# Kernel tuning notes

Hardware: AMD Instinct MI355X
Metric: run time of the kernel (lower is better)

## Reference

```python
import jax, jax.numpy as jnp
import numpy as np

H = 1024
HEADS = 16
FFN = 2048
EPS = 1e-5


def _layernorm(x, g, b):
    mu = jnp.mean(x, axis=-1, keepdims=True)
    var = jnp.mean(jnp.square(x - mu), axis=-1, keepdims=True)
    return (x - mu) * jax.lax.rsqrt(var + EPS) * g + b


def setup_inputs() -> dict:
    key = jax.random.key(0)
    ks = jax.random.split(key, 8)
    N, L = 4, 1024
    s = 1.0 / np.sqrt(H)
    inp = {
        "src_hidden": jax.random.normal(ks[0], (N, L, H), dtype=jnp.float32),
        "src_mask": jnp.ones((N, L), dtype=jnp.int32),
        "Wq": jax.random.normal(ks[1], (H, H), dtype=jnp.float32) * s,
        "bq": jnp.zeros((H,), jnp.float32),
        "Wk": jax.random.normal(ks[2], (H, H), dtype=jnp.float32) * s,
        "bk": jnp.zeros((H,), jnp.float32),
        "Wv": jax.random.normal(ks[3], (H, H), dtype=jnp.float32) * s,
        "bv": jnp.zeros((H,), jnp.float32),
        "Wo": jax.random.normal(ks[4], (H, H), dtype=jnp.float32) * s,
        "bo": jnp.zeros((H,), jnp.float32),
        "ln1_g": jnp.ones((H,), jnp.float32),
        "ln1_b": jnp.zeros((H,), jnp.float32),
        "W1": jax.random.normal(ks[5], (H, FFN), dtype=jnp.float32) * s,
        "b1": jnp.zeros((FFN,), jnp.float32),
        "W2": jax.random.normal(ks[6], (FFN, H), dtype=jnp.float32) * (1.0 / np.sqrt(FFN)),
        "b2": jnp.zeros((H,), jnp.float32),
        "ln2_g": jnp.ones((H,), jnp.float32),
        "ln2_b": jnp.zeros((H,), jnp.float32),
    }
    return inp


def reference(src_hidden, src_mask, Wq, bq, Wk, bk, Wv, bv, Wo, bo,
              ln1_g, ln1_b, W1, b1, W2, b2, ln2_g, ln2_b):
    N, L, _ = src_hidden.shape
    d = H // HEADS
    scale = 1.0 / np.sqrt(H)  # applied to BOTH Q and K, as in the original
    # NOTE: head split is a plain reshape (view), faithful to the original code
    Q = ((src_hidden @ Wq + bq).reshape(N, HEADS, L, d)) * scale
    K = ((src_hidden @ Wk + bk).reshape(N, HEADS, L, d)) * scale
    V = (src_hidden @ Wv + bv).reshape(N, HEADS, L, d)
    sims = jnp.einsum('nhid,nhjd->nhij', Q, K)  # (N, heads, L, L)
    mask = src_mask[:, None, None, :]  # (N,1,1,L) broadcasts over heads and query dim
    sims = jnp.where(mask == 0, -jnp.inf, sims)
    attn = jax.nn.softmax(sims, axis=-1)
    ctx = jnp.einsum('nhij,nhjd->nhid', attn, V)
    concats = ctx.reshape(N, L, H)
    hid = concats @ Wo + bo
    x1 = _layernorm(hid, ln1_g, ln1_b) + hid
    ffn = jax.nn.relu(x1 @ W1 + b1) @ W2 + b2  # dropout is identity in eval
    out = _layernorm(ffn, ln2_g, ln2_b) + ffn
    return (out, src_mask)
```

## Files before the change

kernel.cpp:

```cpp
#include <hip/hip_runtime.h>
#include <math.h>

#define H 1024
#define HEADS 16
#define DH 64
#define FFN_DIM 2048
#define EPS 1e-5f
#define NB 4
#define LL 1024
#define M_ROWS 4096

typedef __attribute__((ext_vector_type(8))) short bf16x8;
typedef __attribute__((ext_vector_type(4))) float f32x4;

__device__ __forceinline__ ushort f2bf(float x) {
    union { float f; unsigned u; } c; c.f = x;
    unsigned u = c.u;
    u += 0x7FFFu + ((u >> 16) & 1u);
    return (ushort)(u >> 16);
}

#define GLL(gp, lp)                                                         \
    __builtin_amdgcn_global_load_lds(                                       \
        (const __attribute__((address_space(1))) void*)(gp),                \
        (__attribute__((address_space(3))) void*)(lp), 16, 0, 0)

#define WAITV4() asm volatile("s_waitcnt vmcnt(4)" ::: "memory")
#define WAITV2() asm volatile("s_waitcnt vmcnt(2)" ::: "memory")
#define WAITV0() asm volatile("s_waitcnt vmcnt(0)" ::: "memory")
#define BAR() __builtin_amdgcn_s_barrier()

__global__ __launch_bounds__(512, 6)
void gemm_bf16(const ushort* __restrict__ A, const ushort* __restrict__ Bt,
               const float* __restrict__ bias, float* __restrict__ Cf0,
               float* __restrict__ Cf1, ushort* __restrict__ Cb,
               int M, int N, int K, int relu, int qkv)
{
    __shared__ ushort As[3][128 * 32];
    __shared__ ushort Bs[3][128 * 32];
    const int tid = threadIdx.x;
    const int l = tid & 63, w = tid >> 6;
    const int wr = w >> 2, wc = w & 3;
    const int g = l >> 4, c0 = l & 15;
    const int brow = blockIdx.y * 128, bcol = blockIdx.x * 128;
    const int z = blockIdx.z;
    const int Ksub = K / gridDim.z;
    const int NS = Ksub >> 5;

    const ushort* Abase = A + (size_t)brow * K + (size_t)z * Ksub;
    const ushort* Bbase = Bt + (size_t)bcol * K + (size_t)z * Ksub;

    f32x4 acc[4][2];
    #pragma unroll
    for (int mi = 0; mi < 4; ++mi)
        #pragma unroll
        for (int ni = 0; ni < 2; ++ni)
            acc[mi][ni] = (f32x4)0.0f;

    auto stage = [&](int buf, int k0) {
        const int row = tid >> 2, cp = tid & 3;
        const int c = cp ^ ((row >> 1) & 3);
        const ushort* ga = Abase + (size_t)row * K + k0 + c * 8;
        const ushort* gb = Bbase + (size_t)row * K + k0 + c * 8;
        ushort* la = As[buf] + (size_t)w * 512;
        ushort* lb = Bs[buf] + (size_t)w * 512;
        GLL(ga, la);
        GLL(gb, lb);
    };

    stage(0, 0);
    stage(1, 32);
    int scur = 0;
    for (int t = 0; t < NS; ++t) {
        int snext = scur + 2; if (snext >= 3) snext -= 3;
        if (t + 2 < NS) stage(snext, (t + 2) << 5);
        if (t < NS - 2)       WAITV4();
        else if (t == NS - 2) WAITV2();
        else                  WAITV0();
        BAR();

        bf16x8 af[4], bf[2];
        #pragma unroll
        for (int mi = 0; mi < 4; ++mi) {
            const int row = wr * 64 + mi * 16 + c0;
            const int cc = g ^ ((row >> 1) & 3);
            af[mi] = *(const bf16x8*)&As[scur][row * 32 + cc * 8];
        }
        #pragma unroll
        for (int ni = 0; ni < 2; ++ni) {
            const int row = wc * 32 + ni * 16 + c0;
            const int cc = g ^ ((row >> 1) & 3);
            bf[ni] = *(const bf16x8*)&Bs[scur][row * 32 + cc * 8];
        }
        __builtin_amdgcn_s_setprio(1);
        #pragma unroll
        for (int mi = 0; mi < 4; ++mi)
            #pragma unroll
            for (int ni = 0; ni < 2; ++ni)
                acc[mi][ni] = __builtin_amdgcn_mfma_f32_16x16x32_bf16(
                    af[mi], bf[ni], acc[mi][ni], 0, 0, 0);
        __builtin_amdgcn_s_setprio(0);
        BAR();
        scur = scur + 1 == 3 ? 0 : scur + 1;
    }

    float* Cf = (z == 0) ? Cf0 : Cf1;
    const int colg0 = bcol + wc * 32 + c0;
    const int rbase = brow + wr * 64 + (g << 2);
    const int seg   = qkv ? (bcol >> 10) : 0;
    const int Nw    = qkv ? 1024 : N;
    ushort* outb    = qkv ? (Cb + (size_t)seg * 4194304u) : Cb;
    #pragma unroll
    for (int ni = 0; ni < 2; ++ni) {
        const int colg = colg0 + ni * 16;
        const int colw = qkv ? (colg & 1023) : colg;
        const float bv = (z == 0) ? bias[colg] : 0.0f;
        #pragma unroll
        for (int mi = 0; mi < 4; ++mi) {
            #pragma unroll
            for (int j = 0; j < 4; ++j) {
                float v = acc[mi][ni][j] + bv;
                if (relu) v = fmaxf(v, 0.0f);
                const size_t off = (size_t)(rbase + mi * 16 + j) * Nw + colw;
                if (Cf) Cf[off] = v;
                if (Cb) outb[off] = f2bf(v);
            }
        }
    }
}

__global__ __launch_bounds__(256)
void transpose_qkvo(const float* __restrict__ Wq, const float* __restrict__ Wk,
                    const float* __restrict__ Wv, const float* __restrict__ Wo,
                    ushort* __restrict__ Dq, ushort* __restrict__ Dk,
                    ushort* __restrict__ Dv, ushort* __restrict__ Do_)
{
    const float* W; ushort* D; float sc;
    switch (blockIdx.z) {
        case 0:  W = Wq; D = Dq;  sc = 0.03125f; break;
        case 1:  W = Wk; D = Dk;  sc = 0.03125f; break;
        case 2:  W = Wv; D = Dv;  sc = 1.0f;     break;
        default: W = Wo; D = Do_; sc = 1.0f;     break;
    }
    __shared__ float t[32][33];
    const int n0 = blockIdx.x * 32, k0 = blockIdx.y * 32;
    const int tx = threadIdx.x & 31, ty = threadIdx.x >> 5;
    #pragma unroll
    for (int r = 0; r < 4; ++r)
        t[ty + r * 8][tx] = W[(size_t)(k0 + ty + r * 8) * H + n0 + tx];
    __syncthreads();
    #pragma unroll
    for (int r = 0; r < 4; ++r)
        D[(size_t)(n0 + ty + r * 8) * H + k0 + tx] =
            f2bf(t[tx][ty + r * 8] * sc);
}

__global__ __launch_bounds__(256)
void transpose_to_bf16(const float* __restrict__ W, ushort* __restrict__ Wt,
                       int K, int N, float scale)
{
    __shared__ float t[32][33];
    const int n0 = blockIdx.x * 32, k0 = blockIdx.y * 32;
    const int tx = threadIdx.x & 31, ty = threadIdx.x >> 5;
    #pragma unroll
    for (int r = 0; r < 4; ++r)
        t[ty + r * 8][tx] = W[(size_t)(k0 + ty + r * 8) * N + n0 + tx];
    __syncthreads();
    #pragma unroll
    for (int r = 0; r < 4; ++r)
        Wt[(size_t)(n0 + ty + r * 8) * K + k0 + tx] =
            f2bf(t[tx][ty + r * 8] * scale);
}

__global__ __launch_bounds__(256)
void transpose_v(const ushort* __restrict__ V, ushort* __restrict__ Vt)
{
    const int nh = blockIdx.y, jt = blockIdx.x;
    const size_t base = (size_t)nh << 16;
    __shared__ ushort t[64][68];
    const int tid = threadIdx.x;
    #pragma unroll
    for (int pass = 0; pass < 4; ++pass) {
        const int j = pass * 16 + (tid >> 4);
        const int d0 = (tid & 15) * 4;
        ushort4 v = *(const ushort4*)&V[base + (size_t)(jt * 64 + j) * 64 + d0];
        t[d0 + 0][j] = v.x; t[d0 + 1][j] = v.y;
        t[d0 + 2][j] = v.z; t[d0 + 3][j] = v.w;
    }
    __syncthreads();
    #pragma unroll
    for (int pass = 0; pass < 4; ++pass) {
        const int d = pass * 16 + (tid >> 4);
        const int j0 = (tid & 15) * 4;
        ushort4 o;
        o.x = t[d][j0 + 0]; o.y = t[d][j0 + 1];
        o.z = t[d][j0 + 2]; o.w = t[d][j0 + 3];
        *(ushort4*)&Vt[base + (size_t)d * 1024 + jt * 64 + j0] = o;
    }
}

__global__ __launch_bounds__(256)
void f32_to_bf16(const float* __restrict__ in, ushort* __restrict__ out, int n4)
{
    const int i = blockIdx.x * blockDim.x + threadIdx.x;
    if (i < n4) {
        float4 v = *reinterpret_cast<const float4*>(&in[i * 4]);
        ushort4 o;
        o.x = f2bf(v.x); o.y = f2bf(v.y); o.z = f2bf(v.z); o.w = f2bf(v.w);
        *reinterpret_cast<ushort4*>(&out[i * 4]) = o;
    }
}

__global__ void build_bias_qkv(const float* __restrict__ bq,
                               const float* __restrict__ bk,
                               const float* __restrict__ bv,
                               float* __restrict__ out)
{
    const int i = blockIdx.x * 256 + threadIdx.x;
    if (i >= 3072) return;
    float v;
    if (i < 1024) v = bq[i] * 0.03125f;
    else if (i < 2048) v = bk[i - 1024] * 0.03125f;
    else v = bv[i - 2048];
    out[i] = v;
}

__global__ void mask_flags(const int* __restrict__ mask, int* __restrict__ fl)
{
    const int t = threadIdx.x;
    if (t < NB * 16) {
        const int n = t >> 4, tile = t & 15;
        int any = 0;
        for (int j = 0; j < 64; ++j)
            any |= (mask[n * LL + tile * 64 + j] == 0);
        fl[t] = any;
    }
}

__global__ __launch_bounds__(256)
void attn_mfma(const ushort* __restrict__ Q, const ushort* __restrict__ K,
               const ushort* __restrict__ Vt, const int* __restrict__ mask,
               const int* __restrict__ mflags, ushort* __restrict__ ctx)
{
    const int nh = blockIdx.y;
    const int n  = nh >> 4;
    const int qb = blockIdx.x;
    const size_t hb = (size_t)nh << 16;
    const ushort* Qh = Q + hb;
    const ushort* Kh = K + hb;
    const ushort* Vh = Vt + hb;
    ushort* Ch = ctx + hb;

    __shared__ ushort Ks[2][64 * 64];
    __shared__ ushort Vs[2][64 * 64];
    __shared__ ushort Ps[4][16 * 64];

    const int tid = threadIdx.x;
    const int l = tid & 63, w = tid >> 6;
    const int g = l >> 4, c0 = l & 15;

    unsigned fbits = 0;
    #pragma unroll
    for (int tt = 0; tt < 16; ++tt)
        fbits |= (unsigned)(mflags[n * 16 + tt] != 0) << tt;

    const ushort* qrow = Qh + (size_t)(qb * 64 + w * 16 + c0) * 64;
    const bf16x8 qf0 = *(const bf16x8*)(qrow + g * 8);
    const bf16x8 qf1 = *(const bf16x8*)(qrow + 32 + g * 8);

    f32x4 Oacc[4];
    #pragma unroll
    for (int nd = 0; nd < 4; ++nd) Oacc[nd] = (f32x4)0.0f;
    float lp[4] = {0.0f, 0.0f, 0.0f, 0.0f};

    auto stage = [&](int buf, int t) {
        #pragma unroll
        for (int i = 0; i < 2; ++i) {
            const int slot = i * 256 + tid;
            const int r = slot >> 3, p = slot & 7;
            const int c = p ^ (r & 7);
            const ushort* gk = Kh + (size_t)(t * 64 + r) * 64 + c * 8;
            const ushort* gv = Vh + (size_t)r * 1024 + t * 64 + c * 8;
            ushort* lk = Ks[buf] + (size_t)(i * 256 + w * 64) * 8;
            ushort* lv = Vs[buf] + (size_t)(i * 256 + w * 64) * 8;
            GLL(gk, lk);
            GLL(gv, lv);
        }
    };

    stage(0, 0);
    int cur = 0;
    for (int t = 0; t < 16; ++t) {
        if (t < 15) { stage(cur ^ 1, t + 1); WAITV4(); }
        else        { WAITV0(); }
        BAR();

        f32x4 s[4];
        #pragma unroll
        for (int nb = 0; nb < 4; ++nb) {
            s[nb] = (f32x4)0.0f;
            const int row = nb * 16 + c0;
            const int cc0 = g ^ (row & 7);
            const int cc1 = (4 + g) ^ (row & 7);
            bf16x8 kf0 = *(const bf16x8*)&Ks[cur][row * 64 + cc0 * 8];
            bf16x8 kf1 = *(const bf16x8*)&Ks[cur][row * 64 + cc1 * 8];
            __builtin_amdgcn_s_setprio(1);
            s[nb] = __builtin_amdgcn_mfma_f32_16x16x32_bf16(qf0, kf0, s[nb], 0, 0, 0);
            s[nb] = __builtin_amdgcn_mfma_f32_16x16x32_bf16(qf1, kf1, s[nb], 0, 0, 0);
            __builtin_amdgcn_s_setprio(0);
        }
        if (fbits >> t & 1) {
            #pragma unroll
            for (int nb = 0; nb < 4; ++nb) {
                const float mb =
                    mask[n * LL + t * 64 + nb * 16 + c0] ? 0.0f : -INFINITY;
                #pragma unroll
                for (int jr = 0; jr < 4; ++jr) s[nb][jr] += mb;
            }
        }
        #pragma unroll
        for (int nb = 0; nb < 4; ++nb)
            #pragma unroll
            for (int jr = 0; jr < 4; ++jr) {
                const float pv = __expf(s[nb][jr]);
                s[nb][jr] = pv;
                lp[jr] += pv;
            }

        ushort* Pw = Ps[w];
        #pragma unroll
        for (int nb = 0; nb < 4; ++nb) {
            const int chunkL = nb * 2 + (c0 >> 3);
            #pragma unroll
            for (int jr = 0; jr < 4; ++jr) {
                const int row = g * 4 + jr;
                const int pch = chunkL ^ (row & 7);
                Pw[row * 64 + pch * 8 + (c0 & 7)] = f2bf(s[nb][jr]);
            }
        }
        const bf16x8 pa0 = *(const bf16x8*)&Pw[c0 * 64 + ((g) ^ (c0 & 7)) * 8];
        const bf16x8 pa1 = *(const bf16x8*)&Pw[c0 * 64 + ((4 + g) ^ (c0 & 7)) * 8];
        #pragma unroll
        for (int nd = 0; nd < 4; ++nd) {
            const int row = nd * 16 + c0;
            const int cc0 = g ^ (row & 7);
            const int cc1 = (4 + g) ^ (row & 7);
            bf16x8 vf0 = *(const bf16x8*)&Vs[cur][row * 64 + cc0 * 8];
            bf16x8 vf1 = *(const bf16x8*)&Vs[cur][row * 64 + cc1 * 8];
            __builtin_amdgcn_s_setprio(1);
            Oacc[nd] = __builtin_amdgcn_mfma_f32_16x16x32_bf16(pa0, vf0, Oacc[nd], 0, 0, 0);
            Oacc[nd] = __builtin_amdgcn_mfma_f32_16x16x32_bf16(pa1, vf1, Oacc[nd], 0, 0, 0);
            __builtin_amdgcn_s_setprio(0);
        }
        BAR();
        cur ^= 1;
    }

    float inv[4];
    #pragma unroll
    for (int jr = 0; jr < 4; ++jr) {
        float v = lp[jr];
        #pragma unroll
        for (int off = 1; off < 16; off <<= 1) v += __shfl_xor(v, off, 64);
        inv[jr] = 1.0f / v;
    }
    #pragma unroll
    for (int nd = 0; nd < 4; ++nd) {
        #pragma unroll
        for (int jr = 0; jr < 4; ++jr) {
            const int row = qb * 64 + w * 16 + g * 4 + jr;
            Ch[(size_t)row * 64 + nd * 16 + c0] = f2bf(Oacc[nd][jr] * inv[jr]);
        }
    }
}

__global__ __launch_bounds__(256)
void ln_residual(const float* __restrict__ X, const float* __restrict__ X2,
                 const float* __restrict__ g, const float* __restrict__ b,
                 float* __restrict__ outf, ushort* __restrict__ outb)
{
    const int row = blockIdx.x;
    const int tid = threadIdx.x;
    float4 xv = *reinterpret_cast<const float4*>(&X[(size_t)row * H + tid * 4]);
    if (X2) {
        float4 yv = *reinterpret_cast<const float4*>(&X2[(size_t)row * H + tid * 4]);
        xv.x += yv.x; xv.y += yv.y; xv.z += yv.z; xv.w += yv.w;
    }
    float s = xv.x + xv.y + xv.z + xv.w;
    __shared__ float red[8];
    const int lane = tid & 63, wave = tid >> 6;
    #pragma unroll
    for (int off = 32; off > 0; off >>= 1) s += __shfl_down(s, off);
    if (lane == 0) red[wave] = s;
    __syncthreads();
    if (tid == 0)
        red[0] = (red[0] + red[1] + red[2] + red[3]) * (1.0f / H);
    __syncthreads();
    const float mu = red[0];
    const float d0 = xv.x - mu, d1 = xv.y - mu, d2 = xv.z - mu, d3 = xv.w - mu;
    float s2 = d0 * d0 + d1 * d1 + d2 * d2 + d3 * d3;
    #pragma unroll
    for (int off = 32; off > 0; off >>= 1) s2 += __shfl_down(s2, off);
    if (lane == 0) red[4 + wave] = s2;
    __syncthreads();
    if (tid == 0) {
        const float var = (red[4] + red[5] + red[6] + red[7]) * (1.0f / H);
        red[4] = rsqrtf(var + EPS);
    }
    __syncthreads();
    const float rstd = red[4];
    float4 gv = *reinterpret_cast<const float4*>(&g[tid * 4]);
    float4 bv = *reinterpret_cast<const float4*>(&b[tid * 4]);
    float4 ov;
    ov.x = d0 * rstd * gv.x + bv.x + xv.x;
    ov.y = d1 * rstd * gv.y + bv.y + xv.y;
    ov.z = d2 * rstd * gv.z + bv.z + xv.z;
    ov.w = d3 * rstd * gv.w + bv.w + xv.w;
    if (outf)
        *reinterpret_cast<float4*>(&outf[(size_t)row * H + tid * 4]) = ov;
    if (outb) {
        ushort4 ob;
        ob.x = f2bf(ov.x); ob.y = f2bf(ov.y);
        ob.z = f2bf(ov.z); ob.w = f2bf(ov.w);
        *reinterpret_cast<ushort4*>(&outb[(size_t)row * H + tid * 4]) = ob;
    }
}

__global__ void mask_to_float(const int* __restrict__ m, float* __restrict__ o,
                              int n)
{
    const int i = blockIdx.x * blockDim.x + threadIdx.x;
    if (i < n) o[i] = (float)m[i];
}

extern "C" void kernel_launch(void* const* d_in, const int* in_sizes, int n_in,
                              void* d_out, int out_size, void* d_ws, size_t ws_size,
                              hipStream_t stream)
{
    const float* X    = (const float*)d_in[0];
    const int*   mask = (const int*)d_in[1];
    const float* Wq   = (const float*)d_in[2];
    const float* bq   = (const float*)d_in[3];
    const float* Wk   = (const float*)d_in[4];
    const float* bk   = (const float*)d_in[5];
    const float* Wv   = (const float*)d_in[6];
    const float* bv   = (const float*)d_in[7];
    const float* Wo   = (const float*)d_in[8];
    const float* bo   = (const float*)d_in[9];
    const float* g1   = (const float*)d_in[10];
    const float* bln1 = (const float*)d_in[11];
    const float* W1   = (const float*)d_in[12];
    const float* b1   = (const float*)d_in[13];
    const float* W2   = (const float*)d_in[14];
    const float* b2   = (const float*)d_in[15];
    const float* g2   = (const float*)d_in[16];
    const float* bln2 = (const float*)d_in[17];

    char* wsb = (char*)d_ws;
    const size_t MB = 1u << 20;
    ushort* Qb16 = (ushort*)(wsb);
    ushort* Vb16 = (ushort*)(wsb + 16 * MB);
    ushort* Xb   = (ushort*)(wsb + 24 * MB);
    ushort* ctxb = (ushort*)(wsb + 24 * MB);
    ushort* Vtb  = (ushort*)(wsb + 32 * MB);
    ushort* Wqkvt = (ushort*)(wsb + 40 * MB);
    ushort* Wot   = (ushort*)(wsb + 46 * MB);
    ushort* W1t   = (ushort*)(wsb + 40 * MB);
    ushort* W2t   = (ushort*)(wsb + 44 * MB);
    float*  biasqkv = (float*)(wsb + 48 * MB);
    int*    mfl     = (int*)(wsb + 48 * MB + 16384);
    float*  P1      = (float*)(wsb + 48 * MB);
    ushort* Fb      = (ushort*)(wsb + 48 * MB);
    float*  P0  = (float*)(wsb);
    ushort* x1b = (ushort*)(wsb + 16 * MB);
    float*  Q0  = (float*)(wsb);
    float*  Q1  = (float*)(wsb + 24 * MB);

    dim3 blk(256), gblk(512);

    f32_to_bf16<<<dim3(M_ROWS * H / 4 / 256), blk, 0, stream>>>(X, Xb, M_ROWS * H / 4);
    transpose_qkvo<<<dim3(32, 32, 4), blk, 0, stream>>>(
        Wq, Wk, Wv, Wo, Wqkvt, Wqkvt + 1024 * 1024, Wqkvt + 2048 * 1024, Wot);
    build_bias_qkv<<<dim3(12), blk, 0, stream>>>(bq, bk, bv, biasqkv);
    mask_flags<<<dim3(1), dim3(64), 0, stream>>>(mask, mfl);

    gemm_bf16<<<dim3(24, 32, 1), gblk, 0, stream>>>(
        Xb, Wqkvt, biasqkv, nullptr, nullptr, Qb16, M_ROWS, 3072, H, 0, 1);
    transpose_v<<<dim3(16, NB * HEADS), blk, 0, stream>>>(Vb16, Vtb);

    attn_mfma<<<dim3(16, NB * HEADS), blk, 0, stream>>>(
        Qb16, Qb16 + 4194304u, Vtb, mask, mfl, ctxb);

    gemm_bf16<<<dim3(8, 32, 2), gblk, 0, stream>>>(
        ctxb, Wot, bo, P0, P1, nullptr, M_ROWS, H, H, 0, 0);
    ln_residual<<<dim3(M_ROWS), blk, 0, stream>>>(P0, P1, g1, bln1, nullptr, x1b);

    transpose_to_bf16<<<dim3(FFN_DIM / 32, H / 32), blk, 0, stream>>>(W1, W1t, H, FFN_DIM, 1.0f);
    transpose_to_bf16<<<dim3(H / 32, FFN_DIM / 32), blk, 0, stream>>>(W2, W2t, FFN_DIM, H, 1.0f);

    gemm_bf16<<<dim3(16, 32, 1), gblk, 0, stream>>>(
        x1b, W1t, b1, nullptr, nullptr, Fb, M_ROWS, FFN_DIM, H, 1, 0);
    gemm_bf16<<<dim3(8, 32, 2), gblk, 0, stream>>>(
        Fb, W2t, b2, Q0, Q1, nullptr, M_ROWS, H, FFN_DIM, 0, 0);

    ln_residual<<<dim3(M_ROWS), blk, 0, stream>>>(Q0, Q1, g2, bln2, (float*)d_out, nullptr);

    mask_to_float<<<dim3((NB * LL + 255) / 256), blk, 0, stream>>>(
        mask, (float*)d_out + (size_t)M_ROWS * H, NB * LL);
}
```

Before: 197.3 us.

## Transpose QK^T MFMA for packed P stores; double-buffer GEMM at higher occupancy

The attention kernel swaps the MFMA operand order so each lane holds four consecutive keys for one query. P can then be packed two bf16 per word and written to LDS as 8-byte stores instead of scalar ushort stores, and the row sum becomes one per-lane accumulator reduced with two shuffles. The conversion to bf16 now uses round-half-up without ties-to-even. Separately, the GEMM drops from triple to double buffering, which cuts LDS use and allows a higher waves-per-EU launch bound, at the cost of less prefetch depth.

```diff
diff --git a/kernel.cpp b/kernel.cpp
--- a/kernel.cpp
+++ b/kernel.cpp
@@ -20,6 +20,13 @@
     return (ushort)(u >> 16);
 }
 
+__device__ __forceinline__ unsigned pack2bf(float a, float b) {
+    union { float f; unsigned u; } ca, cb; ca.f = a; cb.f = b;
+    const unsigned ua = ca.u + 0x8000u;
+    const unsigned ub = cb.u + 0x8000u;
+    return (ua >> 16) | (ub & 0xFFFF0000u);
+}
+
 #define GLL(gp, lp)                                                         \
     __builtin_amdgcn_global_load_lds(                                       \
         (const __attribute__((address_space(1))) void*)(gp),                \
@@ -30,14 +37,14 @@
 #define WAITV0() asm volatile("s_waitcnt vmcnt(0)" ::: "memory")
 #define BAR() __builtin_amdgcn_s_barrier()
 
-__global__ __launch_bounds__(512, 6)
+__global__ __launch_bounds__(512, 8)
 void gemm_bf16(const ushort* __restrict__ A, const ushort* __restrict__ Bt,
                const float* __restrict__ bias, float* __restrict__ Cf0,
                float* __restrict__ Cf1, ushort* __restrict__ Cb,
                int M, int N, int K, int relu, int qkv)
 {
-    __shared__ ushort As[3][128 * 32];
-    __shared__ ushort Bs[3][128 * 32];
+    __shared__ ushort As[2][128 * 32];
+    __shared__ ushort Bs[2][128 * 32];
     const int tid = threadIdx.x;
     const int l = tid & 63, w = tid >> 6;
     const int wr = w >> 2, wc = w & 3;
@@ -69,14 +76,10 @@
     };
 
     stage(0, 0);
-    stage(1, 32);
-    int scur = 0;
+    int cur = 0;
     for (int t = 0; t < NS; ++t) {
-        int snext = scur + 2; if (snext >= 3) snext -= 3;
-        if (t + 2 < NS) stage(snext, (t + 2) << 5);
-        if (t < NS - 2)       WAITV4();
-        else if (t == NS - 2) WAITV2();
-        else                  WAITV0();
+        if (t + 1 < NS) { stage(cur ^ 1, (t + 1) << 5); WAITV2(); }
+        else            { WAITV0(); }
         BAR();
 
         bf16x8 af[4], bf[2];
@@ -84,13 +87,13 @@
         for (int mi = 0; mi < 4; ++mi) {
             const int row = wr * 64 + mi * 16 + c0;
             const int cc = g ^ ((row >> 1) & 3);
-            af[mi] = *(const bf16x8*)&As[scur][row * 32 + cc * 8];
+            af[mi] = *(const bf16x8*)&As[cur][row * 32 + cc * 8];
         }
         #pragma unroll
         for (int ni = 0; ni < 2; ++ni) {
             const int row = wc * 32 + ni * 16 + c0;
             const int cc = g ^ ((row >> 1) & 3);
-            bf[ni] = *(const bf16x8*)&Bs[scur][row * 32 + cc * 8];
+            bf[ni] = *(const bf16x8*)&Bs[cur][row * 32 + cc * 8];
         }
         __builtin_amdgcn_s_setprio(1);
         #pragma unroll
@@ -101,7 +104,7 @@
                     af[mi], bf[ni], acc[mi][ni], 0, 0, 0);
         __builtin_amdgcn_s_setprio(0);
         BAR();
-        scur = scur + 1 == 3 ? 0 : scur + 1;
+        cur ^= 1;
     }
 
     float* Cf = (z == 0) ? Cf0 : Cf1;
@@ -258,6 +261,7 @@
     const int tid = threadIdx.x;
     const int l = tid & 63, w = tid >> 6;
     const int g = l >> 4, c0 = l & 15;
+    const int fsw = (c0 & 7) << 1;
 
     unsigned fbits = 0;
     #pragma unroll
@@ -271,7 +275,7 @@
     f32x4 Oacc[4];
     #pragma unroll
     for (int nd = 0; nd < 4; ++nd) Oacc[nd] = (f32x4)0.0f;
-    float lp[4] = {0.0f, 0.0f, 0.0f, 0.0f};
+    float lp = 0.0f;
 
     auto stage = [&](int buf, int t) {
         #pragma unroll
@@ -305,18 +309,19 @@
             bf16x8 kf0 = *(const bf16x8*)&Ks[cur][row * 64 + cc0 * 8];
             bf16x8 kf1 = *(const bf16x8*)&Ks[cur][row * 64 + cc1 * 8];
             __builtin_amdgcn_s_setprio(1);
-            s[nb] = __builtin_amdgcn_mfma_f32_16x16x32_bf16(qf0, kf0, s[nb], 0, 0, 0);
-            s[nb] = __builtin_amdgcn_mfma_f32_16x16x32_bf16(qf1, kf1, s[nb], 0, 0, 0);
+            s[nb] = __builtin_amdgcn_mfma_f32_16x16x32_bf16(kf0, qf0, s[nb], 0, 0, 0);
+            s[nb] = __builtin_amdgcn_mfma_f32_16x16x32_bf16(kf1, qf1, s[nb], 0, 0, 0);
             __builtin_amdgcn_s_setprio(0);
         }
         if (fbits >> t & 1) {
             #pragma unroll
-            for (int nb = 0; nb < 4; ++nb) {
-                const float mb =
-                    mask[n * LL + t * 64 + nb * 16 + c0] ? 0.0f : -INFINITY;
+            for (int nb = 0; nb < 4; ++nb)
                 #pragma unroll
-                for (int jr = 0; jr < 4; ++jr) s[nb][jr] += mb;
-            }
+                for (int jr = 0; jr < 4; ++jr) {
+                    const int key = 16 * nb + 4 * g + jr;
+                    if (mask[n * LL + t * 64 + key] == 0)
+                        s[nb][jr] = -INFINITY;
+                }
         }
         #pragma unroll
         for (int nb = 0; nb < 4; ++nb)
@@ -324,22 +329,20 @@
             for (int jr = 0; jr < 4; ++jr) {
                 const float pv = __expf(s[nb][jr]);
                 s[nb][jr] = pv;
-                lp[jr] += pv;
+                lp += pv;
             }
 
         ushort* Pw = Ps[w];
         #pragma unroll
         for (int nb = 0; nb < 4; ++nb) {
-            const int chunkL = nb * 2 + (c0 >> 3);
-            #pragma unroll
-            for (int jr = 0; jr < 4; ++jr) {
-                const int row = g * 4 + jr;
-                const int pch = chunkL ^ (row & 7);
-                Pw[row * 64 + pch * 8 + (c0 & 7)] = f2bf(s[nb][jr]);
-            }
-        }
-        const bf16x8 pa0 = *(const bf16x8*)&Pw[c0 * 64 + ((g) ^ (c0 & 7)) * 8];
-        const bf16x8 pa1 = *(const bf16x8*)&Pw[c0 * 64 + ((4 + g) ^ (c0 & 7)) * 8];
+            const int gi = (4 * nb + g) ^ fsw;
+            uint2 pk;
+            pk.x = pack2bf(s[nb][0], s[nb][1]);
+            pk.y = pack2bf(s[nb][2], s[nb][3]);
+            *(uint2*)&Pw[c0 * 64 + gi * 4] = pk;
+        }
+        const bf16x8 pa0 = *(const bf16x8*)&Pw[c0 * 64 + ((2 * g) ^ fsw) * 4];
+        const bf16x8 pa1 = *(const bf16x8*)&Pw[c0 * 64 + ((8 + 2 * g) ^ fsw) * 4];
         #pragma unroll
         for (int nd = 0; nd < 4; ++nd) {
             const int row = nd * 16 + c0;
@@ -356,20 +359,21 @@
         cur ^= 1;
     }
 
-    float inv[4];
+    float v = lp;
+    v += __shfl_xor(v, 16, 64);
+    v += __shfl_xor(v, 32, 64);
+    float invq[4];
     #pragma unroll
     for (int jr = 0; jr < 4; ++jr) {
-        float v = lp[jr];
-        #pragma unroll
-        for (int off = 1; off < 16; off <<= 1) v += __shfl_xor(v, off, 64);
-        inv[jr] = 1.0f / v;
+        const int src = 20 * g + jr;
+        invq[jr] = 1.0f / __shfl(v, src, 64);
     }
     #pragma unroll
     for (int nd = 0; nd < 4; ++nd) {
         #pragma unroll
         for (int jr = 0; jr < 4; ++jr) {
-            const int row = qb * 64 + w * 16 + g * 4 + jr;
-            Ch[(size_t)row * 64 + nd * 16 + c0] = f2bf(Oacc[nd][jr] * inv[jr]);
+            const int row = qb * 64 + w * 16 + 4 * g + jr;
+            Ch[(size_t)row * 64 + nd * 16 + c0] = f2bf(Oacc[nd][jr] * invq[jr]);
         }
     }
 }
```

New measurement: 197.6 us. About the same (+0.1%).
